# Optimization experiments

Hardware: AMD Instinct MI355X
Metric: run time of the kernel (lower is better)

## Reference

```python
import jax, jax.numpy as jnp
import numpy as np

# Model/config constants (match init_kwargs / input_specs)
D_MODEL = 1024
S = 16        # num_signals
N = 4096      # tokens per signal (B*L / S, fully packed)
D_IN = 256    # per-signal encoder embedding_dim
B = 16
L = 4096
MAX_POS = 4096
N_MOD = 4


def setup_inputs() -> dict:
    key = jax.random.key(0)
    ks = jax.random.split(key, 12)
    # Per-signal packed embeddings: emb[s] has shape (N, D_IN)
    emb = jax.random.normal(ks[0], (S, N, D_IN), dtype=jnp.float32)
    # Flat indices (b*L + t); arange partition covers every token slot exactly once
    emb_index = jnp.arange(S * N, dtype=jnp.int32).reshape(S, N)
    pos = jax.random.randint(ks[1], (B, L), 0, MAX_POS)
    sid = jax.random.randint(ks[2], (B, L), 0, S)
    mod = jax.random.randint(ks[3], (B, L), 0, N_MOD)
    role = jax.random.randint(ks[4], (B, L), 0, 2)  # 0=input, 1=actuator
    padding_mask = jnp.zeros((B, L), dtype=bool)     # True = padded
    # Per-signal projection layers nn.Linear(D_IN, D_MODEL): weight (S, D_MODEL, D_IN), bias (S, D_MODEL)
    w_scale = 1.0 / np.sqrt(D_IN)
    W_proj = jax.random.uniform(ks[5], (S, D_MODEL, D_IN), jnp.float32, -w_scale, w_scale)
    b_proj = jax.random.uniform(ks[6], (S, D_MODEL), jnp.float32, -w_scale, w_scale)
    cls_content = jax.random.normal(ks[7], (D_MODEL,), jnp.float32)
    pos_table = jax.random.normal(ks[8], (MAX_POS + 1, D_MODEL), jnp.float32)
    id_table = jax.random.normal(ks[9], (S + 1, D_MODEL), jnp.float32)   # row S = cls_id
    mod_table = jax.random.normal(ks[10], (N_MOD, D_MODEL), jnp.float32)
    role_table = jax.random.normal(ks[11], (3, D_MODEL), jnp.float32)
    return dict(emb=emb, emb_index=emb_index, pos=pos, sid=sid, mod=mod, role=role,
                padding_mask=padding_mask, W_proj=W_proj, b_proj=b_proj,
                cls_content=cls_content, pos_table=pos_table, id_table=id_table,
                mod_table=mod_table, role_table=role_table)


def reference(emb, emb_index, pos, sid, mod, role, padding_mask,
              W_proj, b_proj, cls_content, pos_table, id_table, mod_table, role_table):
    Bd, Ld = pos.shape
    d = cls_content.shape[0]
    # Per-signal linear projection (all S small GEMMs as one batched einsum):
    # proj[s, n, e] = emb[s, n, :] @ W_proj[s].T + b_proj[s]
    proj = jnp.einsum('snd,sed->sne', emb, W_proj) + b_proj[:, None, :]
    # Scatter projected vectors into the flat (B*L, d_model) token grid
    tokens_flat = jnp.zeros((Bd * Ld, d), dtype=proj.dtype)
    tokens_flat = tokens_flat.at[emb_index.reshape(-1)].set(proj.reshape(-1, d))
    tokens = tokens_flat.reshape(Bd, Ld, d)
    # Add metadata embeddings (pos / id / mod / role lookups)
    tokens = tokens + pos_table[pos] + id_table[sid] + mod_table[mod] + role_table[role]
    # Zero out padded positions
    tokens = jnp.where(padding_mask[..., None], jnp.zeros((), tokens.dtype), tokens)
    # Prepend learned CLS token at position 0
    cls = jnp.broadcast_to(cls_content, (Bd, 1, d)).astype(tokens.dtype)
    tokens = jnp.concatenate([cls, tokens], axis=1)          # (B, L+1, d_model)
    attn_keep = jnp.concatenate([jnp.ones((Bd, 1), bool), ~padding_mask], axis=1)
    return tokens, attn_keep
```

## Files before the change

### kernel.cpp

```cpp
#include <hip/hip_runtime.h>
#include <stdint.h>

typedef __attribute__((ext_vector_type(8))) short short8;
typedef __attribute__((ext_vector_type(4))) float f32x4;
typedef unsigned short u16;
typedef unsigned int u32;

#define NSIG   16
#define NPER   4096
#define DIN    256
#define DMODEL 1024
#define NB     16
#define NL     4096
#define LP1    4097
#define LDK    72

__global__ __launch_bounds__(256, 2)
void enc_fused(const float* __restrict__ emb,
               const int* __restrict__ eidx,
               const int* __restrict__ pos,
               const int* __restrict__ sid,
               const int* __restrict__ mod_,
               const int* __restrict__ role,
               const unsigned char* __restrict__ pmask,
               const float* __restrict__ Wp,
               const float* __restrict__ bp,
               const float* __restrict__ pos_t,
               const float* __restrict__ id_t,
               const float* __restrict__ mod_t,
               const float* __restrict__ role_t,
               float* __restrict__ out)
{
    __shared__ u16 Ab[128 * LDK];
    __shared__ u16 Bb[128 * LDK];

    const int bid = blockIdx.x;
    const int lg = (bid & 7) * 512 + (bid >> 3);
    const int rowBase = (lg >> 3) * 128;
    const int colBase = (lg & 7) * 128;
    const int s = rowBase >> 12;

    const int t = threadIdx.x;
    const int lane = t & 63;
    const int w = t >> 6;
    const int wr = w >> 1, wc = w & 1;

    f32x4 acc[4][4] = {};

    const int r0 = t >> 4;
    const int c4 = (t & 15) * 4;

    const float* Ag = emb + (size_t)rowBase * DIN;
    const float* Bg = Wp + ((size_t)s * DMODEL + colBase) * DIN;

    float4 rA[8], rB[8];
    #pragma unroll
    for (int p = 0; p < 8; ++p) {
        const int r = p * 16 + r0;
        rA[p] = *(const float4*)(Ag + (size_t)r * DIN + c4);
        rB[p] = *(const float4*)(Bg + (size_t)r * DIN + c4);
    }

    for (int kk = 0; kk < DIN; kk += 64) {
        #pragma unroll
        for (int p = 0; p < 8; ++p) {
            const int r = p * 16 + r0;
            const float4 va = rA[p];
            const float4 vb = rB[p];
            uint2 pa, pb;
            pa.x = (__builtin_bit_cast(u32, va.x) >> 16) | (__builtin_bit_cast(u32, va.y) & 0xFFFF0000u);
            pa.y = (__builtin_bit_cast(u32, va.z) >> 16) | (__builtin_bit_cast(u32, va.w) & 0xFFFF0000u);
            pb.x = (__builtin_bit_cast(u32, vb.x) >> 16) | (__builtin_bit_cast(u32, vb.y) & 0xFFFF0000u);
            pb.y = (__builtin_bit_cast(u32, vb.z) >> 16) | (__builtin_bit_cast(u32, vb.w) & 0xFFFF0000u);
            *(uint2*)&Ab[r * LDK + c4] = pa;
            *(uint2*)&Bb[r * LDK + c4] = pb;
        }
        __syncthreads();

        if (kk + 64 < DIN) {
            #pragma unroll
            for (int p = 0; p < 8; ++p) {
                const int r = p * 16 + r0;
                rA[p] = *(const float4*)(Ag + (size_t)r * DIN + kk + 64 + c4);
                rB[p] = *(const float4*)(Bg + (size_t)r * DIN + kk + 64 + c4);
            }
        }

        #pragma unroll
        for (int h = 0; h < 2; ++h) {
            const int ko = h * 32 + (lane >> 4) * 8;
            short8 af[4], bf[4];
            #pragma unroll
            for (int m = 0; m < 4; ++m)
                af[m] = *(const short8*)&Ab[(wr * 64 + m * 16 + (lane & 15)) * LDK + ko];
            #pragma unroll
            for (int n = 0; n < 4; ++n)
                bf[n] = *(const short8*)&Bb[(wc * 64 + n * 16 + (lane & 15)) * LDK + ko];
            #pragma unroll
            for (int m = 0; m < 4; ++m) {
                #pragma unroll
                for (int n = 0; n < 4; ++n)
                    acc[m][n] = __builtin_amdgcn_mfma_f32_16x16x32_bf16(
                        af[m], bf[n], acc[m][n], 0, 0, 0);
            }
        }
        __syncthreads();
    }

    const int cb = colBase + wc * 64 + (lane & 15);
    float bpv[4];
    #pragma unroll
    for (int n = 0; n < 4; ++n) bpv[n] = bp[s * DMODEL + cb + n * 16];

    #pragma unroll
    for (int m = 0; m < 4; ++m) {
        #pragma unroll
        for (int j = 0; j < 4; ++j) {
            const int gr = rowBase + wr * 64 + m * 16 + (lane >> 4) * 4 + j;
            const int idx = eidx[gr];
            const int p_ = pos[idx];
            const int si = sid[idx];
            const int mo = mod_[idx];
            const int ro = role[idx];
            const int pm = pmask[idx];
            const size_t orow =
                ((size_t)(idx >> 12) * LP1 + 1 + (size_t)(idx & 4095)) * DMODEL;
            #pragma unroll
            for (int n = 0; n < 4; ++n) {
                const int col = cb + n * 16;
                float v = acc[m][n][j] + bpv[n]
                        + pos_t[(size_t)p_ * DMODEL + col]
                        + id_t[si * DMODEL + col]
                        + mod_t[mo * DMODEL + col]
                        + role_t[ro * DMODEL + col];
                v = pm ? 0.0f : v;
                __builtin_nontemporal_store(v, &out[orow + col]);
            }
        }
    }
}

__global__ void enc_aux(const unsigned char* __restrict__ pmask,
                        const float* __restrict__ cls,
                        float* __restrict__ out)
{
    const size_t OUT_TOK = (size_t)NB * LP1 * DMODEL;
    const int i = blockIdx.x * blockDim.x + threadIdx.x;
    if (i < NB * LP1) {
        const int b = i / LP1;
        const int r = i - b * LP1;
        float keep = 1.0f;
        if (r > 0) keep = pmask[b * NL + r - 1] ? 0.0f : 1.0f;
        out[OUT_TOK + i] = keep;
    }
    if (i < NB * DMODEL) {
        const int b = i >> 10;
        const int e = i & (DMODEL - 1);
        out[(size_t)b * LP1 * DMODEL + e] = cls[e];
    }
}

extern "C" void kernel_launch(void* const* d_in, const int* in_sizes, int n_in,
                              void* d_out, int out_size, void* d_ws, size_t ws_size,
                              hipStream_t stream)
{
    (void)in_sizes; (void)n_in; (void)out_size; (void)d_ws; (void)ws_size;
    const float*         emb    = (const float*)d_in[0];
    const int*           eidx   = (const int*)d_in[1];
    const int*           pos    = (const int*)d_in[2];
    const int*           sid    = (const int*)d_in[3];
    const int*           mod_   = (const int*)d_in[4];
    const int*           role   = (const int*)d_in[5];
    const unsigned char* pmask  = (const unsigned char*)d_in[6];
    const float*         Wp     = (const float*)d_in[7];
    const float*         bp     = (const float*)d_in[8];
    const float*         cls    = (const float*)d_in[9];
    const float*         pos_t  = (const float*)d_in[10];
    const float*         id_t   = (const float*)d_in[11];
    const float*         mod_t  = (const float*)d_in[12];
    const float*         role_t = (const float*)d_in[13];
    float* out = (float*)d_out;

    enc_fused<<<4096, 256, 0, stream>>>(emb, eidx, pos, sid, mod_, role, pmask,
                                        Wp, bp, pos_t, id_t, mod_t, role_t, out);

    const int naux = NB * LP1;
    enc_aux<<<(naux + 255) / 256, 256, 0, stream>>>(pmask, cls, out);
}
```

Before: 129.2 us.

## Shrink K-step to 32, raise occupancy, fold aux kernel into main GEMM kernel

The GEMM K-tile is halved from 64 to 32, which shrinks LDS per block and the register prefetch buffers from 8 to 4 float4 per operand. Launch bounds move from 2 to 6 blocks per SM so more wavefronts can hide memory latency in the gather-heavy epilogue. The separate aux kernel, which writes the attn_keep mask and the CLS rows, is merged into the tail of the fused kernel to remove a launch. In exchange there are twice as many barriers and K iterations, and register pressure may cause spills under the tighter bound.

```diff
diff --git a/kernel.cpp b/kernel.cpp
--- a/kernel.cpp
+++ b/kernel.cpp
@@ -13,9 +13,9 @@
 #define NB     16
 #define NL     4096
 #define LP1    4097
-#define LDK    72
+#define LDK32  40
 
-__global__ __launch_bounds__(256, 2)
+__global__ __launch_bounds__(256, 6)
 void enc_fused(const float* __restrict__ emb,
                const int* __restrict__ eidx,
                const int* __restrict__ pos,
@@ -25,14 +25,15 @@
                const unsigned char* __restrict__ pmask,
                const float* __restrict__ Wp,
                const float* __restrict__ bp,
+               const float* __restrict__ cls,
                const float* __restrict__ pos_t,
                const float* __restrict__ id_t,
                const float* __restrict__ mod_t,
                const float* __restrict__ role_t,
                float* __restrict__ out)
 {
-    __shared__ u16 Ab[128 * LDK];
-    __shared__ u16 Bb[128 * LDK];
+    __shared__ u16 Ab[128 * LDK32];
+    __shared__ u16 Bb[128 * LDK32];
 
     const int bid = blockIdx.x;
     const int lg = (bid & 7) * 512 + (bid >> 3);
@@ -44,27 +45,28 @@
     const int lane = t & 63;
     const int w = t >> 6;
     const int wr = w >> 1, wc = w & 1;
+    const int l4 = lane >> 4;
 
     f32x4 acc[4][4] = {};
 
-    const int r0 = t >> 4;
-    const int c4 = (t & 15) * 4;
+    const int r0 = t >> 3;
+    const int c4f = (t & 7) * 4;
 
     const float* Ag = emb + (size_t)rowBase * DIN;
     const float* Bg = Wp + ((size_t)s * DMODEL + colBase) * DIN;
 
-    float4 rA[8], rB[8];
+    float4 rA[4], rB[4];
     #pragma unroll
-    for (int p = 0; p < 8; ++p) {
-        const int r = p * 16 + r0;
-        rA[p] = *(const float4*)(Ag + (size_t)r * DIN + c4);
-        rB[p] = *(const float4*)(Bg + (size_t)r * DIN + c4);
+    for (int p = 0; p < 4; ++p) {
+        const int r = p * 32 + r0;
+        rA[p] = *(const float4*)(Ag + (size_t)r * DIN + c4f);
+        rB[p] = *(const float4*)(Bg + (size_t)r * DIN + c4f);
     }
 
-    for (int kk = 0; kk < DIN; kk += 64) {
+    for (int kk = 0; kk < DIN; kk += 32) {
         #pragma unroll
-        for (int p = 0; p < 8; ++p) {
-            const int r = p * 16 + r0;
+        for (int p = 0; p < 4; ++p) {
+            const int r = p * 32 + r0;
             const float4 va = rA[p];
             const float4 vb = rB[p];
             uint2 pa, pb;
@@ -72,30 +74,29 @@
             pa.y = (__builtin_bit_cast(u32, va.z) >> 16) | (__builtin_bit_cast(u32, va.w) & 0xFFFF0000u);
             pb.x = (__builtin_bit_cast(u32, vb.x) >> 16) | (__builtin_bit_cast(u32, vb.y) & 0xFFFF0000u);
             pb.y = (__builtin_bit_cast(u32, vb.z) >> 16) | (__builtin_bit_cast(u32, vb.w) & 0xFFFF0000u);
-            *(uint2*)&Ab[r * LDK + c4] = pa;
-            *(uint2*)&Bb[r * LDK + c4] = pb;
+            *(uint2*)&Ab[r * LDK32 + c4f] = pa;
+            *(uint2*)&Bb[r * LDK32 + c4f] = pb;
         }
         __syncthreads();
 
-        if (kk + 64 < DIN) {
+        if (kk + 32 < DIN) {
             #pragma unroll
-            for (int p = 0; p < 8; ++p) {
-                const int r = p * 16 + r0;
-                rA[p] = *(const float4*)(Ag + (size_t)r * DIN + kk + 64 + c4);
-                rB[p] = *(const float4*)(Bg + (size_t)r * DIN + kk + 64 + c4);
+            for (int p = 0; p < 4; ++p) {
+                const int r = p * 32 + r0;
+                rA[p] = *(const float4*)(Ag + (size_t)r * DIN + kk + 32 + c4f);
+                rB[p] = *(const float4*)(Bg + (size_t)r * DIN + kk + 32 + c4f);
             }
         }
 
-        #pragma unroll
-        for (int h = 0; h < 2; ++h) {
-            const int ko = h * 32 + (lane >> 4) * 8;
+        {
+            const int ko = l4 * 8;
             short8 af[4], bf[4];
             #pragma unroll
             for (int m = 0; m < 4; ++m)
-                af[m] = *(const short8*)&Ab[(wr * 64 + m * 16 + (lane & 15)) * LDK + ko];
+                af[m] = *(const short8*)&Ab[(wr * 64 + m * 16 + (lane & 15)) * LDK32 + ko];
             #pragma unroll
             for (int n = 0; n < 4; ++n)
-                bf[n] = *(const short8*)&Bb[(wc * 64 + n * 16 + (lane & 15)) * LDK + ko];
+                bf[n] = *(const short8*)&Bb[(wc * 64 + n * 16 + (lane & 15)) * LDK32 + ko];
             #pragma unroll
             for (int m = 0; m < 4; ++m) {
                 #pragma unroll
@@ -116,7 +117,7 @@
     for (int m = 0; m < 4; ++m) {
         #pragma unroll
         for (int j = 0; j < 4; ++j) {
-            const int gr = rowBase + wr * 64 + m * 16 + (lane >> 4) * 4 + j;
+            const int gr = rowBase + wr * 64 + m * 16 + l4 * 4 + j;
             const int idx = eidx[gr];
             const int p_ = pos[idx];
             const int si = sid[idx];
@@ -138,24 +139,19 @@
             }
         }
     }
-}
 
-__global__ void enc_aux(const unsigned char* __restrict__ pmask,
-                        const float* __restrict__ cls,
-                        float* __restrict__ out)
-{
-    const size_t OUT_TOK = (size_t)NB * LP1 * DMODEL;
-    const int i = blockIdx.x * blockDim.x + threadIdx.x;
-    if (i < NB * LP1) {
-        const int b = i / LP1;
-        const int r = i - b * LP1;
+    const int gid = bid * 256 + t;
+    if (gid < NB * LP1) {
+        const size_t OUT_TOK = (size_t)NB * LP1 * DMODEL;
+        const int b = gid / LP1;
+        const int r = gid - b * LP1;
         float keep = 1.0f;
         if (r > 0) keep = pmask[b * NL + r - 1] ? 0.0f : 1.0f;
-        out[OUT_TOK + i] = keep;
+        out[OUT_TOK + gid] = keep;
     }
-    if (i < NB * DMODEL) {
-        const int b = i >> 10;
-        const int e = i & (DMODEL - 1);
+    if (gid < NB * DMODEL) {
+        const int b = gid >> 10;
+        const int e = gid & (DMODEL - 1);
         out[(size_t)b * LP1 * DMODEL + e] = cls[e];
     }
 }
@@ -182,8 +178,5 @@
     float* out = (float*)d_out;
 
     enc_fused<<<4096, 256, 0, stream>>>(emb, eidx, pos, sid, mod_, role, pmask,
-                                        Wp, bp, pos_t, id_t, mod_t, role_t, out);
-
-    const int naux = NB * LP1;
-    enc_aux<<<(naux + 255) / 256, 256, 0, stream>>>(pmask, cls, out);
+                                        Wp, bp, cls, pos_t, id_t, mod_t, role_t, out);
 }
```

Result: slower. 414.9 us (+221.1%).
